# Kernel tuning notes

Measured on AMD Instinct MI355X. Metric: run time of the kernel, lower is better.

Reference implementation:

```python
import jax, jax.numpy as jnp
import numpy as np
import math

L, B, S, D, DK = 12, 2, 2048, 1024, 256
LN_EPS = 1e-5


def setup_inputs() -> dict:
    key = jax.random.key(0)
    k0, k1, k2 = jax.random.split(key, 3)
    states = jax.random.normal(k0, (L, B, S, D), dtype=jnp.float32)
    # nn.Linear default init ~ U(-1/sqrt(fan_in), 1/sqrt(fan_in))
    bound = 1.0 / math.sqrt(D)
    Wq = jax.random.uniform(k1, (DK, D), minval=-bound, maxval=bound, dtype=jnp.float32)
    Wk = jax.random.uniform(k2, (DK, D), minval=-bound, maxval=bound, dtype=jnp.float32)
    ln_weight = jnp.ones((D,), dtype=jnp.float32)
    ln_bias = jnp.zeros((D,), dtype=jnp.float32)
    latest_gate = jnp.asarray(0.5, dtype=jnp.float32)
    return {"states": states, "Wq": Wq, "Wk": Wk,
            "ln_weight": ln_weight, "ln_bias": ln_bias,
            "latest_gate": latest_gate}


def _layer_norm(x, w, b):
    mu = jnp.mean(x, axis=-1, keepdims=True)
    var = jnp.mean(jnp.square(x - mu), axis=-1, keepdims=True)
    return (x - mu) * jax.lax.rsqrt(var + LN_EPS) * w + b


def reference(states, Wq, Wk, ln_weight, ln_bias, latest_gate):
    # states: (L, B, S, D)
    normalized = _layer_norm(states, ln_weight, ln_bias)          # (L,B,S,D)
    latest = normalized[-1]                                       # (B,S,D)
    query = jnp.einsum('bsd,kd->bsk', latest, Wq)                 # (B,S,DK)
    keys = jnp.einsum('lbsd,kd->lbsk', normalized, Wk)            # (L,B,S,DK)
    scale = 1.0 / math.sqrt(query.shape[-1])
    logits = jnp.einsum('bsk,lbsk->lbs', query, keys) * scale     # (L,B,S)
    weights = jax.nn.softmax(logits, axis=0)                      # softmax over depth
    mixed = jnp.einsum('lbs,lbsd->bsd', weights, states)          # (B,S,D)
    gate = jax.nn.sigmoid(latest_gate)
    return gate * states[-1] + (1.0 - gate) * mixed
```

## Files before the change

kernel.cpp:

```cpp
#include <hip/hip_runtime.h>

#define NL 12
#define NB 2
#define NS 2048
#define ND 1024
#define NDK 256
#define NBS (NB*NS)

typedef __attribute__((ext_vector_type(8))) short short8;
typedef __attribute__((ext_vector_type(4))) float floatx4;

__device__ __forceinline__ unsigned short f2bf(float f) {
    unsigned int u = __float_as_uint(f);
    u += 0x7FFFu + ((u >> 16) & 1u);
    return (unsigned short)(u >> 16);
}
__device__ __forceinline__ short f2bfs(float f) { return (short)f2bf(f); }

__global__ void k_prep_ln(const float* __restrict__ Wq, const float* __restrict__ Wk,
                          const float* __restrict__ x11,
                          const float* __restrict__ lnw, const float* __restrict__ lnb,
                          unsigned short* __restrict__ W2t, unsigned short* __restrict__ U) {
    const int tid = threadIdx.x;
    if (blockIdx.x < 256) {
        const int lane = tid & 63, wv = tid >> 6;
        const int wid = blockIdx.x * 4 + wv;
        const int tm = wid >> 4;
        const int tnb = wid & 15;
        const int lr = lane & 15, kh = lane >> 4;
        floatx4 acc[4];
#pragma unroll
        for (int c = 0; c < 4; ++c) acc[c] = (floatx4){0.f, 0.f, 0.f, 0.f};
#pragma unroll 2
        for (int kb = 0; kb < 8; ++kb) {
            const float* Ab = Wk + (size_t)(kb * 32 + kh * 8) * ND + tm * 16 + lr;
            const float* Bb = Wq + (size_t)(kb * 32 + kh * 8) * ND + tnb * 64 + lr;
            short8 a;
#pragma unroll
            for (int j = 0; j < 8; ++j) a[j] = f2bfs(Ab[(size_t)j * ND]);
#pragma unroll
            for (int c = 0; c < 4; ++c) {
                short8 b;
#pragma unroll
                for (int j = 0; j < 8; ++j) b[j] = f2bfs(Bb[(size_t)j * ND + c * 16]);
                acc[c] = __builtin_amdgcn_mfma_f32_16x16x32_bf16(a, b, acc[c], 0, 0, 0);
            }
        }
#pragma unroll
        for (int c = 0; c < 4; ++c)
#pragma unroll
            for (int r = 0; r < 4; ++r)
                W2t[(size_t)(tm * 16 + kh * 4 + r) * ND + tnb * 64 + c * 16 + lr] = f2bf(acc[c][r]);
        return;
    }
    __shared__ float red[8];
    const int p = blockIdx.x - 256;
    const float4* xr = (const float4*)(x11 + (size_t)p * ND);
    float4 x = xr[tid];
    float s1 = x.x + x.y + x.z + x.w;
    float s2 = x.x*x.x + x.y*x.y + x.z*x.z + x.w*x.w;
#pragma unroll
    for (int m = 32; m > 0; m >>= 1) { s1 += __shfl_xor(s1, m); s2 += __shfl_xor(s2, m); }
    int wv = tid >> 6;
    if ((tid & 63) == 0) { red[wv] = s1; red[4 + wv] = s2; }
    __syncthreads();
    float S1 = red[0] + red[1] + red[2] + red[3];
    float S2 = red[4] + red[5] + red[6] + red[7];
    float mu = S1 * (1.0f / ND);
    float var = S2 * (1.0f / ND) - mu * mu;
    float rstd = rsqrtf(var + 1e-5f);
    float4 w = ((const float4*)lnw)[tid];
    float4 b = ((const float4*)lnb)[tid];
    ushort4 u;
    u.x = f2bf((x.x - mu) * rstd * w.x + b.x);
    u.y = f2bf((x.y - mu) * rstd * w.y + b.y);
    u.z = f2bf((x.z - mu) * rstd * w.z + b.z);
    u.w = f2bf((x.w - mu) * rstd * w.w + b.w);
    ((ushort4*)U)[(size_t)p * (ND / 4) + tid] = u;
}

#define BM 128
#define BN 128
#define BK 64
#define LDP 72
__global__ __launch_bounds__(256) void k_vgemm(const unsigned short* __restrict__ U,
                                               const unsigned short* __restrict__ W2t,
                                               float* __restrict__ V) {
    __shared__ short8 AsV[(BM * LDP) / 8];
    __shared__ short8 BsV[(BN * LDP) / 8];
    unsigned short* As = (unsigned short*)AsV;
    unsigned short* Bs = (unsigned short*)BsV;
    const int tid = threadIdx.x;
    const int lane = tid & 63;
    const int wv = tid >> 6;
    const int wr = wv >> 1, wc = wv & 1;
    const int lr = lane & 15, kh = lane >> 4;
    const int bm0 = (blockIdx.x >> 3) * BM;
    const int bn0 = (blockIdx.x & 7) * BN;
    const int srow = tid >> 1, shalf = tid & 1;
    const short8* gA = (const short8*)(U   + (size_t)(bm0 + srow) * ND + shalf * 32);
    const short8* gB = (const short8*)(W2t + (size_t)(bn0 + srow) * ND + shalf * 32);
    const int sBase = srow * LDP + shalf * 32;

    floatx4 acc[4][4];
#pragma unroll
    for (int m = 0; m < 4; ++m)
#pragma unroll
        for (int n = 0; n < 4; ++n) acc[m][n] = (floatx4){0.f, 0.f, 0.f, 0.f};

    short8 ra[4], rb[4];
#pragma unroll
    for (int j = 0; j < 4; ++j) { ra[j] = gA[j]; rb[j] = gB[j]; }

    const int NT = 1024 / BK;
#pragma unroll 1
    for (int t = 0; t < NT; ++t) {
        __syncthreads();
#pragma unroll
        for (int j = 0; j < 4; ++j) {
            *(short8*)&As[sBase + j * 8] = ra[j];
            *(short8*)&Bs[sBase + j * 8] = rb[j];
        }
        __syncthreads();
        if (t < NT - 1) {
#pragma unroll
            for (int j = 0; j < 4; ++j) { ra[j] = gA[(t + 1) * 8 + j]; rb[j] = gB[(t + 1) * 8 + j]; }
        }
#pragma unroll
        for (int kk = 0; kk < 2; ++kk) {
            short8 a[4], b[4];
#pragma unroll
            for (int m = 0; m < 4; ++m)
                a[m] = *(const short8*)&As[(wr * 64 + m * 16 + lr) * LDP + kk * 32 + kh * 8];
#pragma unroll
            for (int n = 0; n < 4; ++n)
                b[n] = *(const short8*)&Bs[(wc * 64 + n * 16 + lr) * LDP + kk * 32 + kh * 8];
#pragma unroll
            for (int m = 0; m < 4; ++m)
#pragma unroll
                for (int n = 0; n < 4; ++n)
                    acc[m][n] = __builtin_amdgcn_mfma_f32_16x16x32_bf16(a[m], b[n], acc[m][n], 0, 0, 0);
        }
    }
#pragma unroll
    for (int m = 0; m < 4; ++m)
#pragma unroll
        for (int n = 0; n < 4; ++n)
#pragma unroll
            for (int r = 0; r < 4; ++r)
                V[(size_t)(bm0 + wr * 64 + m * 16 + kh * 4 + r) * ND + bn0 + wc * 64 + n * 16 + lr]
                    = acc[m][n][r];
}

__global__ void k_fused(const float* __restrict__ states, const float* __restrict__ V,
                        const float* __restrict__ lnw, const float* __restrict__ lnb,
                        const float* __restrict__ gatep, float* __restrict__ out) {
    __shared__ float s_logit[12];
    __shared__ float s_w12[12];
    __shared__ float s_g;
    __shared__ float s_part[4][ND];
    __shared__ float s_x11[ND];
    const int p = blockIdx.x;
    const int tid = threadIdx.x;
    const int lane = tid & 63;
    const int wv = tid >> 6;
    const size_t LS = (size_t)NBS * ND;
    const float* base = states + (size_t)p * ND;
    const float4* Vp = (const float4*)(V + (size_t)p * ND);

    float4 t[4];
    float red[11];
#pragma unroll
    for (int j = 0; j < 11; ++j) red[j] = 0.f;
#pragma unroll
    for (int i = 0; i < 4; ++i) {
        int idx = lane + 64 * i;
        float4 v = Vp[idx];
        float4 w = ((const float4*)lnw)[idx];
        float4 b = ((const float4*)lnb)[idx];
        float4 tt; tt.x = v.x*w.x; tt.y = v.y*w.y; tt.z = v.z*w.z; tt.w = v.w*w.w;
        t[i] = tt;
        red[9]  += tt.x + tt.y + tt.z + tt.w;
        red[10] += v.x*b.x + v.y*b.y + v.z*b.z + v.w*b.w;
    }

    float4 x[3][4];
#pragma unroll
    for (int rr = 0; rr < 3; ++rr) {
        const int l = wv + 4 * rr;
        const float4* xr = (const float4*)(base + (size_t)l * LS);
#pragma unroll
        for (int i = 0; i < 4; ++i) {
            float4 xx = xr[lane + 64 * i];
            x[rr][i] = xx;
            red[rr]     += xx.x + xx.y + xx.z + xx.w;
            red[3 + rr] += xx.x*xx.x + xx.y*xx.y + xx.z*xx.z + xx.w*xx.w;
            red[6 + rr] += xx.x*t[i].x + xx.y*t[i].y + xx.z*t[i].z + xx.w*t[i].w;
        }
    }
#pragma unroll
    for (int m = 32; m > 0; m >>= 1) {
#pragma unroll
        for (int j = 0; j < 11; ++j) red[j] += __shfl_xor(red[j], m);
    }
    if (lane == 0) {
#pragma unroll
        for (int rr = 0; rr < 3; ++rr) {
            float mu = red[rr] * (1.0f / ND);
            float var = red[3 + rr] * (1.0f / ND) - mu * mu;
            float rstd = rsqrtf(var + 1e-5f);
            s_logit[wv + 4 * rr] = 0.0625f * (rstd * (red[6 + rr] - mu * red[9]) + red[10]);
        }
    }
    __syncthreads();
    if (tid == 0) {
        float mx = s_logit[0];
#pragma unroll
        for (int l = 1; l < 12; ++l) mx = fmaxf(mx, s_logit[l]);
        float e[12], sum = 0.f;
#pragma unroll
        for (int l = 0; l < 12; ++l) { e[l] = expf(s_logit[l] - mx); sum += e[l]; }
        float inv = 1.0f / sum;
#pragma unroll
        for (int l = 0; l < 12; ++l) s_w12[l] = e[l] * inv;
        s_g = 1.0f / (1.0f + expf(-gatep[0]));
    }
    __syncthreads();

    const float w0 = s_w12[wv], w1 = s_w12[wv + 4], w2 = s_w12[wv + 8];
#pragma unroll
    for (int i = 0; i < 4; ++i) {
        int idx = lane + 64 * i;
        float4 pm;
        pm.x = w0*x[0][i].x + w1*x[1][i].x + w2*x[2][i].x;
        pm.y = w0*x[0][i].y + w1*x[1][i].y + w2*x[2][i].y;
        pm.z = w0*x[0][i].z + w1*x[1][i].z + w2*x[2][i].z;
        pm.w = w0*x[0][i].w + w1*x[1][i].w + w2*x[2][i].w;
        ((float4*)s_part[wv])[idx] = pm;
        if (wv == 3) ((float4*)s_x11)[idx] = x[2][i];
    }
    __syncthreads();

    const float g = s_g;
    float4 a0 = ((const float4*)s_part[0])[tid];
    float4 a1 = ((const float4*)s_part[1])[tid];
    float4 a2 = ((const float4*)s_part[2])[tid];
    float4 a3 = ((const float4*)s_part[3])[tid];
    float4 x11 = ((const float4*)s_x11)[tid];
    float4 o;
    o.x = g * x11.x + (1.f - g) * (a0.x + a1.x + a2.x + a3.x);
    o.y = g * x11.y + (1.f - g) * (a0.y + a1.y + a2.y + a3.y);
    o.z = g * x11.z + (1.f - g) * (a0.z + a1.z + a2.z + a3.z);
    o.w = g * x11.w + (1.f - g) * (a0.w + a1.w + a2.w + a3.w);
    ((float4*)(out + (size_t)p * ND))[tid] = o;
}

extern "C" void kernel_launch(void* const* d_in, const int* in_sizes, int n_in,
                              void* d_out, int out_size, void* d_ws, size_t ws_size,
                              hipStream_t stream) {
    (void)in_sizes; (void)n_in; (void)out_size; (void)ws_size;
    const float* states = (const float*)d_in[0];
    const float* Wq     = (const float*)d_in[1];
    const float* Wk     = (const float*)d_in[2];
    const float* lnw    = (const float*)d_in[3];
    const float* lnb    = (const float*)d_in[4];
    const float* gate   = (const float*)d_in[5];
    float* out = (float*)d_out;
    char* ws = (char*)d_ws;

    unsigned short* U   = (unsigned short*)(ws);
    unsigned short* W2t = (unsigned short*)(ws + (9u << 20));
    float*          V   = (float*)        (ws + (12u << 20));

    k_prep_ln<<<dim3(256 + NBS), dim3(256), 0, stream>>>(
        Wq, Wk, states + (size_t)(NL - 1) * NBS * ND, lnw, lnb, W2t, U);
    k_vgemm<<<dim3((NBS / BM) * (ND / BN)), dim3(256), 0, stream>>>(U, W2t, V);
    k_fused<<<dim3(NBS), dim3(256), 0, stream>>>(states, V, lnw, lnb, gate, out);
}
```

Baseline: 77.09 us.

## Store intermediate V in bf16 and halve GEMM M-tile to 64

The intermediate V matrix written by the GEMM and read by the fused kernel is now stored as bf16 instead of fp32, halving that round-trip traffic. The GEMM M-tile shrinks from 128 to 64 rows, doubling the block count to 512 for better CU occupancy on the 4096x1024 output, and the global-to-shared load mapping is reorganised to match. Rounding V to bf16 adds error to the logits that feed the depth softmax.

```diff
diff --git a/kernel.cpp b/kernel.cpp
--- a/kernel.cpp
+++ b/kernel.cpp
@@ -8,6 +8,7 @@
 #define NBS (NB*NS)
 
 typedef __attribute__((ext_vector_type(8))) short short8;
+typedef __attribute__((ext_vector_type(4))) short short4v;
 typedef __attribute__((ext_vector_type(4))) float floatx4;
 
 __device__ __forceinline__ unsigned short f2bf(float f) {
@@ -16,6 +17,9 @@
     return (unsigned short)(u >> 16);
 }
 __device__ __forceinline__ short f2bfs(float f) { return (short)f2bf(f); }
+__device__ __forceinline__ float bf2f(short s) {
+    return __uint_as_float(((unsigned int)(unsigned short)s) << 16);
+}
 
 __global__ void k_prep_ln(const float* __restrict__ Wq, const float* __restrict__ Wk,
                           const float* __restrict__ x11,
@@ -79,13 +83,13 @@
     ((ushort4*)U)[(size_t)p * (ND / 4) + tid] = u;
 }
 
-#define BM 128
+#define BM 64
 #define BN 128
 #define BK 64
 #define LDP 72
 __global__ __launch_bounds__(256) void k_vgemm(const unsigned short* __restrict__ U,
                                                const unsigned short* __restrict__ W2t,
-                                               float* __restrict__ V) {
+                                               unsigned short* __restrict__ V) {
     __shared__ short8 AsV[(BM * LDP) / 8];
     __shared__ short8 BsV[(BN * LDP) / 8];
     unsigned short* As = (unsigned short*)AsV;
@@ -97,62 +101,83 @@
     const int lr = lane & 15, kh = lane >> 4;
     const int bm0 = (blockIdx.x >> 3) * BM;
     const int bn0 = (blockIdx.x & 7) * BN;
-    const int srow = tid >> 1, shalf = tid & 1;
-    const short8* gA = (const short8*)(U   + (size_t)(bm0 + srow) * ND + shalf * 32);
-    const short8* gB = (const short8*)(W2t + (size_t)(bn0 + srow) * ND + shalf * 32);
-    const int sBase = srow * LDP + shalf * 32;
-
-    floatx4 acc[4][4];
-#pragma unroll
-    for (int m = 0; m < 4; ++m)
+
+    int aRow[2], aOff[2];
+#pragma unroll
+    for (int j = 0; j < 2; ++j) {
+        int idx = j * 256 + tid;
+        aRow[j] = idx >> 3;
+        aOff[j] = (idx >> 3) * LDP + (idx & 7) * 8;
+    }
+    int bRow[4], bOff[4];
+#pragma unroll
+    for (int j = 0; j < 4; ++j) {
+        int idx = j * 256 + tid;
+        bRow[j] = idx >> 3;
+        bOff[j] = (idx >> 3) * LDP + (idx & 7) * 8;
+    }
+    const short8* gA[2]; const short8* gB[4];
+#pragma unroll
+    for (int j = 0; j < 2; ++j)
+        gA[j] = (const short8*)(U + (size_t)(bm0 + aRow[j]) * ND) + ((aOff[j] - aRow[j] * LDP) >> 3);
+#pragma unroll
+    for (int j = 0; j < 4; ++j)
+        gB[j] = (const short8*)(W2t + (size_t)(bn0 + bRow[j]) * ND) + ((bOff[j] - bRow[j] * LDP) >> 3);
+
+    floatx4 acc[2][4];
+#pragma unroll
+    for (int m = 0; m < 2; ++m)
 #pragma unroll
         for (int n = 0; n < 4; ++n) acc[m][n] = (floatx4){0.f, 0.f, 0.f, 0.f};
 
-    short8 ra[4], rb[4];
-#pragma unroll
-    for (int j = 0; j < 4; ++j) { ra[j] = gA[j]; rb[j] = gB[j]; }
-
-    const int NT = 1024 / BK;
+    short8 ra[2], rb[4];
+#pragma unroll
+    for (int j = 0; j < 2; ++j) ra[j] = gA[j][0];
+#pragma unroll
+    for (int j = 0; j < 4; ++j) rb[j] = gB[j][0];
+
+    const int NT = ND / BK;
 #pragma unroll 1
     for (int t = 0; t < NT; ++t) {
         __syncthreads();
 #pragma unroll
-        for (int j = 0; j < 4; ++j) {
-            *(short8*)&As[sBase + j * 8] = ra[j];
-            *(short8*)&Bs[sBase + j * 8] = rb[j];
-        }
+        for (int j = 0; j < 2; ++j) *(short8*)&As[aOff[j]] = ra[j];
+#pragma unroll
+        for (int j = 0; j < 4; ++j) *(short8*)&Bs[bOff[j]] = rb[j];
         __syncthreads();
         if (t < NT - 1) {
 #pragma unroll
-            for (int j = 0; j < 4; ++j) { ra[j] = gA[(t + 1) * 8 + j]; rb[j] = gB[(t + 1) * 8 + j]; }
+            for (int j = 0; j < 2; ++j) ra[j] = gA[j][(t + 1) * 8];
+#pragma unroll
+            for (int j = 0; j < 4; ++j) rb[j] = gB[j][(t + 1) * 8];
         }
 #pragma unroll
         for (int kk = 0; kk < 2; ++kk) {
-            short8 a[4], b[4];
-#pragma unroll
-            for (int m = 0; m < 4; ++m)
-                a[m] = *(const short8*)&As[(wr * 64 + m * 16 + lr) * LDP + kk * 32 + kh * 8];
+            short8 a[2], b[4];
+#pragma unroll
+            for (int m = 0; m < 2; ++m)
+                a[m] = *(const short8*)&As[(wr * 32 + m * 16 + lr) * LDP + kk * 32 + kh * 8];
 #pragma unroll
             for (int n = 0; n < 4; ++n)
                 b[n] = *(const short8*)&Bs[(wc * 64 + n * 16 + lr) * LDP + kk * 32 + kh * 8];
 #pragma unroll
-            for (int m = 0; m < 4; ++m)
+            for (int m = 0; m < 2; ++m)
 #pragma unroll
                 for (int n = 0; n < 4; ++n)
                     acc[m][n] = __builtin_amdgcn_mfma_f32_16x16x32_bf16(a[m], b[n], acc[m][n], 0, 0, 0);
         }
     }
 #pragma unroll
-    for (int m = 0; m < 4; ++m)
+    for (int m = 0; m < 2; ++m)
 #pragma unroll
         for (int n = 0; n < 4; ++n)
 #pragma unroll
             for (int r = 0; r < 4; ++r)
-                V[(size_t)(bm0 + wr * 64 + m * 16 + kh * 4 + r) * ND + bn0 + wc * 64 + n * 16 + lr]
-                    = acc[m][n][r];
-}
-
-__global__ void k_fused(const float* __restrict__ states, const float* __restrict__ V,
+                V[(size_t)(bm0 + wr * 32 + m * 16 + kh * 4 + r) * ND + bn0 + wc * 64 + n * 16 + lr]
+                    = f2bf(acc[m][n][r]);
+}
+
+__global__ void k_fused(const float* __restrict__ states, const unsigned short* __restrict__ V,
                         const float* __restrict__ lnw, const float* __restrict__ lnb,
                         const float* __restrict__ gatep, float* __restrict__ out) {
     __shared__ float s_logit[12];
@@ -166,7 +191,7 @@
     const int wv = tid >> 6;
     const size_t LS = (size_t)NBS * ND;
     const float* base = states + (size_t)p * ND;
-    const float4* Vp = (const float4*)(V + (size_t)p * ND);
+    const short4v* Vp = (const short4v*)(V + (size_t)p * ND);
 
     float4 t[4];
     float red[11];
@@ -175,7 +200,9 @@
 #pragma unroll
     for (int i = 0; i < 4; ++i) {
         int idx = lane + 64 * i;
-        float4 v = Vp[idx];
+        short4v vq = Vp[idx];
+        float4 v;
+        v.x = bf2f(vq[0]); v.y = bf2f(vq[1]); v.z = bf2f(vq[2]); v.w = bf2f(vq[3]);
         float4 w = ((const float4*)lnw)[idx];
         float4 b = ((const float4*)lnb)[idx];
         float4 tt; tt.x = v.x*w.x; tt.y = v.y*w.y; tt.z = v.z*w.z; tt.w = v.w*w.w;
@@ -270,7 +297,7 @@
 
     unsigned short* U   = (unsigned short*)(ws);
     unsigned short* W2t = (unsigned short*)(ws + (9u << 20));
-    float*          V   = (float*)        (ws + (12u << 20));
+    unsigned short* V   = (unsigned short*)(ws + (12u << 20));
 
     k_prep_ln<<<dim3(256 + NBS), dim3(256), 0, stream>>>(
         Wq, Wk, states + (size_t)(NL - 1) * NBS * ND, lnw, lnb, W2t, U);
```

Measured after the change: 75.43 us. 2.2% less time.
